# Kernel tuning notes

Measured on AMD Instinct MI355X. Metric: run time of the kernel, lower is better.

The kernel has to match this reference:

```python
import jax, jax.numpy as jnp
import numpy as np

RES = 64
NU = 0.002
DX = 2.0 * np.pi / RES
DT = 0.001
M1 = 12
M2 = 12
WIDTH = 32


def _central(x, axis, dx):
    # periodic central difference via roll (matches torch.roll semantics)
    return (jnp.roll(x, -1, axis) - jnp.roll(x, 1, axis)) / (2.0 * dx)


def _grad_module(u):
    # TurbulenceRCLN.compute_grad_u: central diff in x,y; j==2 branch is u*0.1 (kept faithfully)
    g0 = _central(u, 2, DX)
    g1 = _central(u, 3, DX)
    g2 = u * 0.1
    return jnp.stack([g0, g1, g2], axis=2)  # (B,3,3,N,N,N) indexed [b,i,j]


def _grad_solver(u):
    # NavierStokesSolver._compute_gradient: true central differences in all 3 dirs
    return jnp.stack([_central(u, 2 + j, DX) for j in range(3)], axis=2)


def _laplacian(u):
    lap = jnp.zeros_like(u)
    for ax in (2, 3, 4):
        lap = lap + (jnp.roll(u, -1, ax) - 2.0 * u + jnp.roll(u, 1, ax)) / (DX * DX)
    return lap


def _div_tau(tau):
    # tau: (B,3,3,N,N,N); div_i = sum_j d tau_ij / dx_j
    return sum(_central(tau[:, :, j], 2 + j, DX) for j in range(3))


def _spectral_conv(x, w1, w2):
    # x: (B,C,N,N); w1/w2: (C,C,M1,M2,2) real/imag
    N = x.shape[-1]
    xft = jnp.fft.rfft2(x)  # (B,C,N,N//2+1) complex
    w1c = w1[..., 0] + 1j * w1[..., 1]
    w2c = w2[..., 0] + 1j * w2[..., 1]
    a = jnp.einsum('bixy,ioxy->boxy', xft[:, :, :M1, :M2], w1c)
    b = jnp.einsum('bixy,ioxy->boxy', xft[:, :, -M1:, :M2], w2c)
    out = jnp.zeros_like(xft).at[:, :, :M1, :M2].set(a).at[:, :, -M1:, :M2].set(b)
    return jnp.fft.irfft2(out, s=(N, N))


def _fno2d(x, fc0_w, fc0_b, spec_w1, spec_w2, conv_w, conv_b, fc1_w, fc1_b, fc2_w, fc2_b):
    h = jnp.einsum('bcxy,cd->bdxy', x, fc0_w) + fc0_b[None, :, None, None]
    for l in range(4):
        s = _spectral_conv(h, spec_w1[l], spec_w2[l])
        w = jnp.einsum('bcxy,co->boxy', h, conv_w[l]) + conv_b[l][None, :, None, None]
        h = s + w
        if l < 3:
            h = jax.nn.gelu(h)
    h = jax.nn.gelu(jnp.einsum('bcxy,cd->bdxy', h, fc1_w) + fc1_b[None, :, None, None])
    return jnp.einsum('bcxy,cd->bdxy', h, fc2_w) + fc2_b[None, :, None, None]


def setup_inputs() -> dict:
    key = jax.random.key(0)
    ks = jax.random.split(key, 8)
    B = 16
    scale = 1.0 / (WIDTH * WIDTH)
    return {
        'velocity': jax.random.normal(ks[0], (B, 3, RES, RES, RES), jnp.float32),
        'fc0_w': jax.random.normal(ks[1], (10, WIDTH), jnp.float32) * 0.1,
        'fc0_b': jnp.zeros((WIDTH,), jnp.float32),
        'spec_w1': jax.random.normal(ks[2], (4, WIDTH, WIDTH, M1, M2, 2), jnp.float32) * scale,
        'spec_w2': jax.random.normal(ks[3], (4, WIDTH, WIDTH, M1, M2, 2), jnp.float32) * scale,
        'conv_w': jax.random.normal(ks[4], (4, WIDTH, WIDTH), jnp.float32) * 0.1,
        'conv_b': jnp.zeros((4, WIDTH), jnp.float32),
        'fc1_w': jax.random.normal(ks[5], (WIDTH, 128), jnp.float32) * 0.1,
        'fc1_b': jnp.zeros((128,), jnp.float32),
        'fc2_w': jax.random.normal(ks[6], (128, 6), jnp.float32) * 0.1,
        'fc2_b': jnp.zeros((6,), jnp.float32),
    }


def reference(velocity, fc0_w, fc0_b, spec_w1, spec_w2, conv_w, conv_b, fc1_w, fc1_b, fc2_w, fc2_b):
    B = velocity.shape[0]
    N = RES
    # --- soft-shell closure input ---
    grad_u = _grad_module(velocity)                                   # (B,3,3,N,N,N)
    S = 0.5 * (grad_u + jnp.swapaxes(grad_u, 1, 2))
    S_mag = jnp.sqrt(2.0 * jnp.sum(S * S, axis=(1, 2), keepdims=True))  # (B,1,1,N,N,N)
    g_slice = grad_u[:, :, :, :, N // 2, :].reshape(B, 9, N, N)        # 9 grad channels at mid-plane
    s_slice = S_mag[:, :, :, :, N // 2, :].reshape(B, 1, N, N)         # 1 strain-mag channel
    closure_in = jnp.concatenate([g_slice, s_slice], axis=1)          # (B,10,N,N)
    tau2d = _fno2d(closure_in, fc0_w, fc0_b, spec_w1, spec_w2, conv_w, conv_b,
                   fc1_w, fc1_b, fc2_w, fc2_b)                         # (B,6,N,N)
    t = jnp.broadcast_to(tau2d[..., None], (B, 6, N, N, N))           # expand along z
    # reconstruct symmetric stress tensor (B,3,3,N,N,N)
    row0 = jnp.stack([t[:, 0], t[:, 3], t[:, 4]], axis=1)
    row1 = jnp.stack([t[:, 3], t[:, 1], t[:, 5]], axis=1)
    row2 = jnp.stack([t[:, 4], t[:, 5], t[:, 2]], axis=1)
    tau_full = jnp.stack([row0, row1, row2], axis=1)
    # --- hard-core NS step ---
    g = _grad_solver(velocity)
    lap = _laplacian(velocity)
    convection = jnp.einsum('bixyz,bijxyz->bjxyz', velocity, g)
    div_tau = _div_tau(tau_full)
    return velocity + DT * (-convection + NU * lap + div_tau)
```

## Files before the change

### kernel.cpp

```cpp
#include <hip/hip_runtime.h>
#include <math.h>

#define NRES 64
#define NXY  4096
#define NVOL 262144
#define BB   16
#define WID  32
#define MM   12
#define R24  24

constexpr double DX_d   = 2.0 * 3.14159265358979323846 / 64.0;
constexpr float  INV2DX = (float)(1.0 / (2.0 * DX_d));
constexpr float  INVDX2 = (float)(1.0 / (DX_d * DX_d));
constexpr float  DT_c   = 0.001f;
constexpr float  NU_c   = 0.002f;

constexpr size_t OFF_FR  = 0;
constexpr size_t OFF_FI  = OFF_FR + (size_t)R24 * NRES;
constexpr size_t OFF_GR  = OFF_FI + (size_t)R24 * NRES;
constexpr size_t OFF_GI  = OFF_GR + (size_t)MM * NRES;
constexpr size_t OFF_CL  = OFF_GI + (size_t)MM * NRES;
constexpr size_t OFF_HA  = OFF_CL + (size_t)BB * 10 * NXY;
constexpr size_t OFF_HB  = OFF_HA + (size_t)BB * WID * NXY;
constexpr size_t OFF_T1R = OFF_HB + (size_t)BB * WID * NXY;
constexpr size_t OFF_T1I = OFF_T1R + (size_t)BB * WID * R24 * NRES;
constexpr size_t OFF_XR  = OFF_T1I + (size_t)BB * WID * R24 * NRES;
constexpr size_t OFF_XI  = OFF_XR + (size_t)BB * WID * R24 * MM;
constexpr size_t OFF_MR  = OFF_XI + (size_t)BB * WID * R24 * MM;
constexpr size_t OFF_MI  = OFF_MR + (size_t)BB * WID * R24 * MM;
constexpr size_t OFF_AR  = OFF_MI + (size_t)BB * WID * R24 * MM;
constexpr size_t OFF_AI  = OFF_AR + (size_t)BB * WID * MM * NRES;
constexpr size_t OFF_H1  = OFF_AI + (size_t)BB * WID * MM * NRES;
constexpr size_t OFF_TAU = OFF_H1 + (size_t)BB * 128 * NXY;
constexpr size_t OFF_FRT = OFF_TAU + (size_t)BB * 6 * NXY;
constexpr size_t OFF_FIT = OFF_FRT + (size_t)NRES * R24;

constexpr size_t OFF_SP  = OFF_H1;
constexpr size_t OFF_W1T = OFF_H1 + (size_t)BB * WID * NXY;
constexpr size_t OFF_CWT = OFF_W1T + 4096;
constexpr size_t OFF_W0T = OFF_CWT + 4096;

__device__ __forceinline__ float gelu_fast(float x) {
    float z = 0.79788456080286535588f * (x + 0.044715f * x * x * x);
    float e = __expf(2.0f * z);
    float t = 1.0f - 2.0f / (e + 1.0f);
    return 0.5f * x * (1.0f + t);
}

__global__ void k_setup(const float* __restrict__ fc1w, const float* __restrict__ convw,
                        const float* __restrict__ fc0w, float* __restrict__ ws) {
    int idx = blockIdx.x * 256 + threadIdx.x;
    if (idx < R24 * NRES) {
        int r = idx / NRES, x = idx % NRES;
        int kx = (r < MM) ? r : (r + 40);
        double ang = -2.0 * 3.14159265358979323846 * (double)(kx * x) / 64.0;
        float cr = (float)cos(ang), ci = (float)sin(ang);
        ws[OFF_FR + idx] = cr;
        ws[OFF_FI + idx] = ci;
        ws[OFF_FRT + (size_t)x * R24 + r] = cr;
        ws[OFF_FIT + (size_t)x * R24 + r] = ci;
    }
    if (idx < MM * NRES) {
        int ky = idx / NRES, y = idx % NRES;
        double ang = -2.0 * 3.14159265358979323846 * (double)(ky * y) / 64.0;
        ws[OFF_GR + idx] = (float)cos(ang);
        ws[OFF_GI + idx] = (float)sin(ang);
    }
    if (idx < 4096) {
        int c = idx >> 7, e = idx & 127;
        ws[OFF_W1T + (size_t)e * 32 + c] = fc1w[idx];
    } else if (idx < 8192) {
        int j = idx - 4096;
        int l = j >> 10, r = j & 1023;
        int c = r >> 5, o = r & 31;
        ws[OFF_CWT + (size_t)l * 1024 + o * 32 + c] = convw[j];
    } else if (idx < 8512) {
        int j = idx - 8192;
        int c = j >> 5, d = j & 31;
        ws[OFF_W0T + (size_t)d * 10 + c] = fc0w[j];
    }
}

__global__ void k_clfc0(const float* __restrict__ v, const float* __restrict__ w0t,
                        const float* __restrict__ bias, float* __restrict__ h) {
    __shared__ __align__(16) float sw[32 * 12];
    __shared__ float sb[32];
    int tid = threadIdx.x;
    for (int i = tid; i < 320; i += 256) {
        int d = i / 10, c = i % 10;
        sw[d * 12 + c] = w0t[i];
    }
    if (tid < 32) sb[tid] = bias[tid];
    __syncthreads();
    int idx = blockIdx.x * 256 + tid;
    int b = idx >> 10;
    int rr = idx & 1023;
    int x = rr >> 4, z0 = (rr & 15) * 4;
    int xp = (x + 1) & 63, xm = (x - 1) & 63;
    float4 cv[10];
    for (int i = 0; i < 3; i++) {
        const float* vb = v + (((size_t)(b * 3 + i)) << 18);
        float4 u4   = *(const float4*)(vb + (size_t)x  * 4096 + 32 * 64 + z0);
        float4 uxp4 = *(const float4*)(vb + (size_t)xp * 4096 + 32 * 64 + z0);
        float4 uxm4 = *(const float4*)(vb + (size_t)xm * 4096 + 32 * 64 + z0);
        float4 uyp4 = *(const float4*)(vb + (size_t)x  * 4096 + 33 * 64 + z0);
        float4 uym4 = *(const float4*)(vb + (size_t)x  * 4096 + 31 * 64 + z0);
        cv[i * 3 + 0] = make_float4((uxp4.x - uxm4.x) * INV2DX, (uxp4.y - uxm4.y) * INV2DX,
                                    (uxp4.z - uxm4.z) * INV2DX, (uxp4.w - uxm4.w) * INV2DX);
        cv[i * 3 + 1] = make_float4((uyp4.x - uym4.x) * INV2DX, (uyp4.y - uym4.y) * INV2DX,
                                    (uyp4.z - uym4.z) * INV2DX, (uyp4.w - uym4.w) * INV2DX);
        cv[i * 3 + 2] = make_float4(0.1f * u4.x, 0.1f * u4.y, 0.1f * u4.z, 0.1f * u4.w);
    }
    float4 ss = make_float4(0.f, 0.f, 0.f, 0.f);
    for (int i = 0; i < 3; i++)
        for (int j = 0; j < 3; j++) {
            float4 a = cv[i * 3 + j], bt = cv[j * 3 + i];
            float sx = 0.5f * (a.x + bt.x), sy = 0.5f * (a.y + bt.y);
            float sz = 0.5f * (a.z + bt.z), sw_ = 0.5f * (a.w + bt.w);
            ss.x += sx * sx; ss.y += sy * sy; ss.z += sz * sz; ss.w += sw_ * sw_;
        }
    cv[9] = make_float4(sqrtf(2.f * ss.x), sqrtf(2.f * ss.y),
                        sqrtf(2.f * ss.z), sqrtf(2.f * ss.w));
    float* hp = h + (size_t)b * WID * NXY + (size_t)x * 64 + z0;
#pragma unroll
    for (int d = 0; d < 32; d++) {
        float4 acc = make_float4(sb[d], sb[d], sb[d], sb[d]);
#pragma unroll
        for (int c = 0; c < 10; c++) {
            float w = sw[d * 12 + c];
            acc.x += w * cv[c].x; acc.y += w * cv[c].y;
            acc.z += w * cv[c].z; acc.w += w * cv[c].w;
        }
        *(float4*)(hp + (size_t)d * NXY) = acc;
    }
}

__global__ void k_fwd(const float* __restrict__ h, const float* __restrict__ ws,
                      float* __restrict__ xr, float* __restrict__ xi) {
    __shared__ __align__(16) float sh[4096];
    __shared__ float st1r[24 * 65];
    __shared__ float st1i[24 * 65];
    int tid = threadIdx.x;
    int bc = blockIdx.x;
    const float4* hp4 = (const float4*)(h + (size_t)bc * NXY);
    float4* sh4 = (float4*)sh;
#pragma unroll
    for (int i = 0; i < 4; i++) sh4[tid + 256 * i] = hp4[tid + 256 * i];
    __syncthreads();
    const float* FRT = ws + OFF_FRT;
    const float* FIT = ws + OFF_FIT;
#pragma unroll
    for (int it = 0; it < 6; it++) {
        int point = it * 256 + tid;
        int y = point & 63;
        int rr = __builtin_amdgcn_readfirstlane(point >> 6);
        float ar = 0.f, ai = 0.f;
#pragma unroll 16
        for (int x = 0; x < 64; x++) {
            float hv = sh[x * 64 + y];
            ar += hv * FRT[x * R24 + rr];
            ai += hv * FIT[x * R24 + rr];
        }
        st1r[rr * 65 + y] = ar;
        st1i[rr * 65 + y] = ai;
    }
    __syncthreads();
    const float* GR = ws + OFF_GR;
    const float* GI = ws + OFF_GI;
#pragma unroll
    for (int it = 0; it < 2; it++) {
        int point = it * 256 + tid;
        if (point < 288) {
            int r = point / 12, ky = point - r * 12;
            const float* Gr = GR + (size_t)ky * 64;
            const float* Gi = GI + (size_t)ky * 64;
            float ar = 0.f, ai = 0.f;
#pragma unroll 16
            for (int y = 0; y < 64; y++) {
                float a = st1r[r * 65 + y], b = st1i[r * 65 + y];
                float c = Gr[y], d = Gi[y];
                ar += a * c - b * d;
                ai += a * d + b * c;
            }
            xr[(size_t)bc * 288 + point] = ar;
            xi[(size_t)bc * 288 + point] = ai;
        }
    }
}

__global__ void k_specinv(const float* __restrict__ xr, const float* __restrict__ xi,
                          const float* __restrict__ w1, const float* __restrict__ w2,
                          const float* __restrict__ ws, float* __restrict__ sp) {
    __shared__ float sm_r[288];
    __shared__ float sm_i[288];
    __shared__ float sa_r[12 * 64];
    __shared__ float sa_i[12 * 64];
    int tid = threadIdx.x;
    int bo = blockIdx.x;
    int o = bo & 31, b = bo >> 5;
    for (int m = tid; m < 288; m += 256) {
        int r = m / 12;
        int kxy = (r < MM) ? m : (m - 144);
        const float* wp = ((r < MM) ? w1 : w2) + ((size_t)o * 144 + kxy) * 2;
        size_t xbase = (size_t)b * 32 * 288 + m;
        float ar = 0.f, ai = 0.f;
#pragma unroll 8
        for (int i = 0; i < 32; i++) {
            float a   = xr[xbase + (size_t)i * 288];
            float bb  = xi[xbase + (size_t)i * 288];
            float wr_ = wp[(size_t)i * 9216];
            float wi_ = wp[(size_t)i * 9216 + 1];
            ar += a * wr_ - bb * wi_;
            ai += a * wi_ + bb * wr_;
        }
        sm_r[m] = ar; sm_i[m] = ai;
    }
    __syncthreads();
    const float* FR = ws + OFF_FR;
    const float* FI = ws + OFF_FI;
#pragma unroll
    for (int it = 0; it < 3; it++) {
        int point = it * 256 + tid;
        int x = point & 63;
        int ky = __builtin_amdgcn_readfirstlane(point >> 6);
        float ar = 0.f, ai = 0.f;
#pragma unroll 8
        for (int r = 0; r < 24; r++) {
            float a = sm_r[r * 12 + ky], bb = sm_i[r * 12 + ky];
            float c = FR[r * 64 + x], d = FI[r * 64 + x];
            ar += a * c + bb * d;
            ai += bb * c - a * d;
        }
        sa_r[ky * 64 + x] = ar;
        sa_i[ky * 64 + x] = ai;
    }
    __syncthreads();
    const float* GR = ws + OFF_GR;
    const float* GI = ws + OFF_GI;
    float* spb = sp + (size_t)bo * NXY;
#pragma unroll
    for (int it = 0; it < 16; it++) {
        int px = it * 256 + tid;
        int y = px & 63;
        int x = __builtin_amdgcn_readfirstlane(px >> 6);
        float s = sa_r[x];
#pragma unroll
        for (int ky = 1; ky < 12; ky++) {
            float gr = GR[ky * 64 + y];
            float gi = GI[ky * 64 + y];
            s += 2.0f * (sa_r[ky * 64 + x] * gr + sa_i[ky * 64 + x] * gi);
        }
        spb[px] = s * (1.0f / 4096.0f);
    }
}

template <int DOGELU>
__global__ void k_convg(const float* __restrict__ sp, const float* __restrict__ hin,
                        const float* __restrict__ cwt, const float* __restrict__ cb,
                        float* __restrict__ hout) {
    __shared__ __align__(16) float scw[1024];
    __shared__ float scb[32];
    int tid = threadIdx.x;
#pragma unroll
    for (int i = 0; i < 4; i++) scw[tid + 256 * i] = cwt[tid + 256 * i];
    if (tid < 32) scb[tid] = cb[tid];
    __syncthreads();
    int wid = tid >> 6, lane = tid & 63;
    int pix = blockIdx.x * 64 + lane;
    int b = pix >> 12, p = pix & 4095;
    const float* hp = hin + (size_t)b * WID * NXY + p;
    float hv[32];
#pragma unroll
    for (int c = 0; c < 32; c++) hv[c] = hp[(size_t)c * NXY];
    const float* spp = sp + (size_t)b * WID * NXY + p;
    float* op = hout + (size_t)b * WID * NXY + p;
#pragma unroll
    for (int j = 0; j < 8; j++) {
        int o = wid * 8 + j;
        const float4* wr = (const float4*)&scw[o * 32];
        float a0 = 0.f, a1 = 0.f, a2 = 0.f, a3 = 0.f;
#pragma unroll
        for (int q = 0; q < 8; q += 4) {
            float4 w0 = wr[q], w1 = wr[q + 1], w2 = wr[q + 2], w3 = wr[q + 3];
            a0 += w0.x * hv[q * 4]      + w0.y * hv[q * 4 + 1]  + w0.z * hv[q * 4 + 2]  + w0.w * hv[q * 4 + 3];
            a1 += w1.x * hv[q * 4 + 4]  + w1.y * hv[q * 4 + 5]  + w1.z * hv[q * 4 + 6]  + w1.w * hv[q * 4 + 7];
            a2 += w2.x * hv[q * 4 + 8]  + w2.y * hv[q * 4 + 9]  + w2.z * hv[q * 4 + 10] + w2.w * hv[q * 4 + 11];
            a3 += w3.x * hv[q * 4 + 12] + w3.y * hv[q * 4 + 13] + w3.z * hv[q * 4 + 14] + w3.w * hv[q * 4 + 15];
        }
        float v = scb[o] + (a0 + a1) + (a2 + a3) + spp[(size_t)o * NXY];
        if (DOGELU) v = gelu_fast(v);
        op[(size_t)o * NXY] = v;
    }
}

__global__ void k_head(const float* __restrict__ h, const float* __restrict__ w1t,
                       const float* __restrict__ b1, const float* __restrict__ w2,
                       const float* __restrict__ b2, float* __restrict__ tau) {
    __shared__ __align__(16) float sw1[4096];
    __shared__ float sb1[128];
    __shared__ __align__(16) float sw2[128 * 8];
    __shared__ float red[4][6][64];
    int tid = threadIdx.x;
#pragma unroll
    for (int i = 0; i < 16; i++) sw1[tid + 256 * i] = w1t[tid + 256 * i];
    if (tid < 128) sb1[tid] = b1[tid];
    for (int i = tid; i < 768; i += 256) {
        int e = i / 6, t = i - e * 6;
        sw2[e * 8 + t] = w2[i];
    }
    __syncthreads();
    int wid = tid >> 6, lane = tid & 63;
    int pix = blockIdx.x * 64 + lane;
    int b = pix >> 12, p = pix & 4095;
    const float* hp = h + (size_t)b * WID * NXY + p;
    float hv[32];
#pragma unroll
    for (int c = 0; c < 32; c++) hv[c] = hp[(size_t)c * NXY];
    float acc[6] = {0.f, 0.f, 0.f, 0.f, 0.f, 0.f};
#pragma unroll
    for (int jj = 0; jj < 32; jj++) {
        int e = wid * 32 + jj;
        const float4* wr = (const float4*)&sw1[e * 32];
        float d0 = 0.f, d1 = 0.f, d2 = 0.f, d3 = 0.f;
#pragma unroll
        for (int q = 0; q < 8; q += 4) {
            float4 w0 = wr[q], w1 = wr[q + 1], w2_ = wr[q + 2], w3 = wr[q + 3];
            d0 += w0.x * hv[q * 4]      + w0.y * hv[q * 4 + 1]  + w0.z * hv[q * 4 + 2]  + w0.w * hv[q * 4 + 3];
            d1 += w1.x * hv[q * 4 + 4]  + w1.y * hv[q * 4 + 5]  + w1.z * hv[q * 4 + 6]  + w1.w * hv[q * 4 + 7];
            d2 += w2_.x * hv[q * 4 + 8] + w2_.y * hv[q * 4 + 9] + w2_.z * hv[q * 4 + 10]+ w2_.w * hv[q * 4 + 11];
            d3 += w3.x * hv[q * 4 + 12] + w3.y * hv[q * 4 + 13] + w3.z * hv[q * 4 + 14] + w3.w * hv[q * 4 + 15];
        }
        float d = sb1[e] + (d0 + d1) + (d2 + d3);
        float g = gelu_fast(d);
        const float4* w2r = (const float4*)&sw2[e * 8];
        float4 wa = w2r[0], wb = w2r[1];
        acc[0] += g * wa.x; acc[1] += g * wa.y; acc[2] += g * wa.z;
        acc[3] += g * wa.w; acc[4] += g * wb.x; acc[5] += g * wb.y;
    }
#pragma unroll
    for (int t = 0; t < 6; t++) red[wid][t][lane] = acc[t];
    __syncthreads();
    if (wid == 0) {
        float* tb = tau + (size_t)b * 6 * NXY + p;
#pragma unroll
        for (int t = 0; t < 6; t++)
            tb[(size_t)t * NXY] = red[0][t][lane] + red[1][t][lane] +
                                  red[2][t][lane] + red[3][t][lane] + b2[t];
    }
}

__global__ void k_ns(const float* __restrict__ v, const float* __restrict__ tau,
                     float* __restrict__ out) {
    int idx = blockIdx.x * 256 + threadIdx.x;
    int b = idx >> 16;
    int r = idx & 65535;
    int x = r >> 10;
    int y = (r >> 4) & 63;
    int z0 = (r & 15) * 4;
    int xp = (x + 1) & 63, xm = (x - 1) & 63;
    int yp = (y + 1) & 63, ym = (y - 1) & 63;
    int zm = (z0 - 1) & 63, zp = (z0 + 4) & 63;

    float4 u[3], gx[3], gy[3], gz[3], lap[3];
    for (int i = 0; i < 3; i++) {
        const float* vb = v + (((size_t)(b * 3 + i)) << 18);
        const float* row = vb + (size_t)x * 4096 + (size_t)y * 64;
        float4 c4   = *(const float4*)(row + z0);
        float  czm  = row[zm];
        float  czp  = row[zp];
        float4 xp4  = *(const float4*)(vb + (size_t)xp * 4096 + (size_t)y * 64 + z0);
        float4 xm4  = *(const float4*)(vb + (size_t)xm * 4096 + (size_t)y * 64 + z0);
        float4 yp4  = *(const float4*)(vb + (size_t)x * 4096 + (size_t)yp * 64 + z0);
        float4 ym4  = *(const float4*)(vb + (size_t)x * 4096 + (size_t)ym * 64 + z0);
        u[i] = c4;
        gx[i] = make_float4((xp4.x - xm4.x) * INV2DX, (xp4.y - xm4.y) * INV2DX,
                            (xp4.z - xm4.z) * INV2DX, (xp4.w - xm4.w) * INV2DX);
        gy[i] = make_float4((yp4.x - ym4.x) * INV2DX, (yp4.y - ym4.y) * INV2DX,
                            (yp4.z - ym4.z) * INV2DX, (yp4.w - ym4.w) * INV2DX);
        gz[i] = make_float4((c4.y - czm) * INV2DX, (c4.z - c4.x) * INV2DX,
                            (c4.w - c4.y) * INV2DX, (czp - c4.z) * INV2DX);
        lap[i] = make_float4(
            (xp4.x + xm4.x + yp4.x + ym4.x + czm  + c4.y - 6.f * c4.x) * INVDX2,
            (xp4.y + xm4.y + yp4.y + ym4.y + c4.x + c4.z - 6.f * c4.y) * INVDX2,
            (xp4.z + xm4.z + yp4.z + ym4.z + c4.y + c4.w - 6.f * c4.z) * INVDX2,
            (xp4.w + xm4.w + yp4.w + ym4.w + c4.z + czp  - 6.f * c4.w) * INVDX2);
    }
    const float* tb = tau + (size_t)b * 6 * NXY;
    int pxp = xp * 64 + y, pxm = xm * 64 + y, pyp = x * 64 + yp, pym = x * 64 + ym;
    float d0 = (tb[0 * NXY + pxp] - tb[0 * NXY + pxm]) * INV2DX +
               (tb[3 * NXY + pyp] - tb[3 * NXY + pym]) * INV2DX;
    float d1 = (tb[3 * NXY + pxp] - tb[3 * NXY + pxm]) * INV2DX +
               (tb[1 * NXY + pyp] - tb[1 * NXY + pym]) * INV2DX;
    float d2 = (tb[4 * NXY + pxp] - tb[4 * NXY + pxm]) * INV2DX +
               (tb[5 * NXY + pyp] - tb[5 * NXY + pym]) * INV2DX;

    size_t so = ((size_t)b * 3) * NVOL + (size_t)x * 4096 + (size_t)y * 64 + z0;
#pragma unroll
    for (int i = 0; i < 3; i++) {
        float dti = (i == 0) ? d0 : (i == 1) ? d1 : d2;
        float4 conv = make_float4(
            u[0].x * ((i==0)?gx[0].x:(i==1)?gy[0].x:gz[0].x) + u[1].x * ((i==0)?gx[1].x:(i==1)?gy[1].x:gz[1].x) + u[2].x * ((i==0)?gx[2].x:(i==1)?gy[2].x:gz[2].x),
            u[0].y * ((i==0)?gx[0].y:(i==1)?gy[0].y:gz[0].y) + u[1].y * ((i==0)?gx[1].y:(i==1)?gy[1].y:gz[1].y) + u[2].y * ((i==0)?gx[2].y:(i==1)?gy[2].y:gz[2].y),
            u[0].z * ((i==0)?gx[0].z:(i==1)?gy[0].z:gz[0].z) + u[1].z * ((i==0)?gx[1].z:(i==1)?gy[1].z:gz[1].z) + u[2].z * ((i==0)?gx[2].z:(i==1)?gy[2].z:gz[2].z),
            u[0].w * ((i==0)?gx[0].w:(i==1)?gy[0].w:gz[0].w) + u[1].w * ((i==0)?gx[1].w:(i==1)?gy[1].w:gz[1].w) + u[2].w * ((i==0)?gx[2].w:(i==1)?gy[2].w:gz[2].w));
        float4 res = make_float4(
            u[i].x + DT_c * (-conv.x + NU_c * lap[i].x + dti),
            u[i].y + DT_c * (-conv.y + NU_c * lap[i].y + dti),
            u[i].z + DT_c * (-conv.z + NU_c * lap[i].z + dti),
            u[i].w + DT_c * (-conv.w + NU_c * lap[i].w + dti));
        *(float4*)(out + so + (size_t)i * NVOL) = res;
    }
}

extern "C" void kernel_launch(void* const* d_in, const int* in_sizes, int n_in,
                              void* d_out, int out_size, void* d_ws, size_t ws_size,
                              hipStream_t stream) {
    const float* vel   = (const float*)d_in[0];
    const float* fc0w  = (const float*)d_in[1];
    const float* fc0b  = (const float*)d_in[2];
    const float* sw1   = (const float*)d_in[3];
    const float* sw2   = (const float*)d_in[4];
    const float* convw = (const float*)d_in[5];
    const float* convb = (const float*)d_in[6];
    const float* fc1w  = (const float*)d_in[7];
    const float* fc1b  = (const float*)d_in[8];
    const float* fc2w  = (const float*)d_in[9];
    const float* fc2b  = (const float*)d_in[10];
    float* ws  = (float*)d_ws;
    float* out = (float*)d_out;

    k_setup<<<34, 256, 0, stream>>>(fc1w, convw, fc0w, ws);
    k_clfc0<<<64, 256, 0, stream>>>(vel, ws + OFF_W0T, fc0b, ws + OFF_HA);

    float* hcur  = ws + OFF_HA;
    float* hnext = ws + OFF_HB;
    for (int l = 0; l < 4; l++) {
        const float* wl1 = sw1 + (size_t)l * WID * WID * MM * MM * 2;
        const float* wl2 = sw2 + (size_t)l * WID * WID * MM * MM * 2;
        const float* cwl = ws + OFF_CWT + (size_t)l * WID * WID;
        const float* cbl = convb + (size_t)l * WID;
        k_fwd<<<512, 256, 0, stream>>>(hcur, ws, ws + OFF_XR, ws + OFF_XI);
        k_specinv<<<512, 256, 0, stream>>>(ws + OFF_XR, ws + OFF_XI, wl1, wl2, ws, ws + OFF_SP);
        if (l < 3)
            k_convg<1><<<1024, 256, 0, stream>>>(ws + OFF_SP, hcur, cwl, cbl, hnext);
        else
            k_convg<0><<<1024, 256, 0, stream>>>(ws + OFF_SP, hcur, cwl, cbl, hnext);
        float* tmp = hcur; hcur = hnext; hnext = tmp;
    }

    k_head<<<1024, 256, 0, stream>>>(hcur, ws + OFF_W1T, fc1b, fc2w, fc2b, ws + OFF_TAU);
    k_ns<<<4096, 256, 0, stream>>>(vel, ws + OFF_TAU, out);
}
```

Baseline: 249.2 us.

## Register-block FNO kernels over four pixels and four modes per thread

The 1x1 conv and head kernels now have each thread handle four adjacent pixels using float4 loads and stores. Each shared-memory weight read is therefore reused four times, and the grid shrinks fourfold. The forward DFT computes four frequency rows per thread, reusing each loaded input value. The inverse DFT keeps the mode coefficients in registers and writes float4 outputs. The cost is much higher register use (128 floats for hv in conv and head), which lowers occupancy and leaves only 256 blocks, which may underfill the GPU.

After: 718.9 us. +188.5%, slower.

```diff
diff --git a/kernel.cpp b/kernel.cpp
--- a/kernel.cpp
+++ b/kernel.cpp
@@ -47,6 +47,10 @@
     return 0.5f * x * (1.0f + t);
 }
 
+__device__ __forceinline__ float4 gelu4(float4 v) {
+    return make_float4(gelu_fast(v.x), gelu_fast(v.y), gelu_fast(v.z), gelu_fast(v.w));
+}
+
 __global__ void k_setup(const float* __restrict__ fc1w, const float* __restrict__ convw,
                         const float* __restrict__ fc0w, float* __restrict__ ws) {
     int idx = blockIdx.x * 256 + threadIdx.x;
@@ -149,20 +153,26 @@
     __syncthreads();
     const float* FRT = ws + OFF_FRT;
     const float* FIT = ws + OFF_FIT;
-#pragma unroll
-    for (int it = 0; it < 6; it++) {
-        int point = it * 256 + tid;
-        int y = point & 63;
-        int rr = __builtin_amdgcn_readfirstlane(point >> 6);
-        float ar = 0.f, ai = 0.f;
-#pragma unroll 16
+    int y = tid & 63;
+    int wid = tid >> 6;
+    for (int g = wid; g < 6; g += 4) {
+        int r0 = __builtin_amdgcn_readfirstlane(g * 4);
+        float ar0 = 0.f, ai0 = 0.f, ar1 = 0.f, ai1 = 0.f;
+        float ar2 = 0.f, ai2 = 0.f, ar3 = 0.f, ai3 = 0.f;
+#pragma unroll 8
         for (int x = 0; x < 64; x++) {
             float hv = sh[x * 64 + y];
-            ar += hv * FRT[x * R24 + rr];
-            ai += hv * FIT[x * R24 + rr];
-        }
-        st1r[rr * 65 + y] = ar;
-        st1i[rr * 65 + y] = ai;
+            const float* fr = FRT + x * R24 + r0;
+            const float* fi = FIT + x * R24 + r0;
+            ar0 += hv * fr[0]; ai0 += hv * fi[0];
+            ar1 += hv * fr[1]; ai1 += hv * fi[1];
+            ar2 += hv * fr[2]; ai2 += hv * fi[2];
+            ar3 += hv * fr[3]; ai3 += hv * fi[3];
+        }
+        st1r[(r0 + 0) * 65 + y] = ar0; st1i[(r0 + 0) * 65 + y] = ai0;
+        st1r[(r0 + 1) * 65 + y] = ar1; st1i[(r0 + 1) * 65 + y] = ai1;
+        st1r[(r0 + 2) * 65 + y] = ar2; st1i[(r0 + 2) * 65 + y] = ai2;
+        st1r[(r0 + 3) * 65 + y] = ar3; st1i[(r0 + 3) * 65 + y] = ai3;
     }
     __syncthreads();
     const float* GR = ws + OFF_GR;
@@ -176,9 +186,9 @@
             const float* Gi = GI + (size_t)ky * 64;
             float ar = 0.f, ai = 0.f;
 #pragma unroll 16
-            for (int y = 0; y < 64; y++) {
-                float a = st1r[r * 65 + y], b = st1i[r * 65 + y];
-                float c = Gr[y], d = Gi[y];
+            for (int yy = 0; yy < 64; yy++) {
+                float a = st1r[r * 65 + yy], b = st1i[r * 65 + yy];
+                float c = Gr[yy], d = Gi[yy];
                 ar += a * c - b * d;
                 ai += a * d + b * c;
             }
@@ -238,19 +248,31 @@
     const float* GR = ws + OFF_GR;
     const float* GI = ws + OFF_GI;
     float* spb = sp + (size_t)bo * NXY;
-#pragma unroll
-    for (int it = 0; it < 16; it++) {
-        int px = it * 256 + tid;
-        int y = px & 63;
-        int x = __builtin_amdgcn_readfirstlane(px >> 6);
-        float s = sa_r[x];
+    int x = tid >> 2, ys = (tid & 3) * 16;
+    float a0 = sa_r[x];
+    float arv[11], aiv[11];
+#pragma unroll
+    for (int ky = 1; ky < 12; ky++) {
+        arv[ky - 1] = sa_r[ky * 64 + x];
+        aiv[ky - 1] = sa_i[ky * 64 + x];
+    }
+#pragma unroll
+    for (int j = 0; j < 4; j++) {
+        int y0 = ys + j * 4;
+        float4 s = make_float4(a0, a0, a0, a0);
 #pragma unroll
         for (int ky = 1; ky < 12; ky++) {
-            float gr = GR[ky * 64 + y];
-            float gi = GI[ky * 64 + y];
-            s += 2.0f * (sa_r[ky * 64 + x] * gr + sa_i[ky * 64 + x] * gi);
-        }
-        spb[px] = s * (1.0f / 4096.0f);
+            float4 g4r = *(const float4*)(GR + ky * 64 + y0);
+            float4 g4i = *(const float4*)(GI + ky * 64 + y0);
+            float ar = arv[ky - 1], ai = aiv[ky - 1];
+            s.x += 2.0f * (ar * g4r.x + ai * g4i.x);
+            s.y += 2.0f * (ar * g4r.y + ai * g4i.y);
+            s.z += 2.0f * (ar * g4r.z + ai * g4i.z);
+            s.w += 2.0f * (ar * g4r.w + ai * g4i.w);
+        }
+        s.x *= (1.0f / 4096.0f); s.y *= (1.0f / 4096.0f);
+        s.z *= (1.0f / 4096.0f); s.w *= (1.0f / 4096.0f);
+        *(float4*)(spb + (size_t)x * 64 + y0) = s;
     }
 }
 
@@ -266,30 +288,32 @@
     if (tid < 32) scb[tid] = cb[tid];
     __syncthreads();
     int wid = tid >> 6, lane = tid & 63;
-    int pix = blockIdx.x * 64 + lane;
-    int b = pix >> 12, p = pix & 4095;
+    int q = blockIdx.x * 64 + lane;
+    int b = q >> 10, p = (q & 1023) * 4;
     const float* hp = hin + (size_t)b * WID * NXY + p;
-    float hv[32];
-#pragma unroll
-    for (int c = 0; c < 32; c++) hv[c] = hp[(size_t)c * NXY];
+    float4 hv[32];
+#pragma unroll
+    for (int c = 0; c < 32; c++) hv[c] = *(const float4*)(hp + (size_t)c * NXY);
     const float* spp = sp + (size_t)b * WID * NXY + p;
     float* op = hout + (size_t)b * WID * NXY + p;
 #pragma unroll
     for (int j = 0; j < 8; j++) {
         int o = wid * 8 + j;
         const float4* wr = (const float4*)&scw[o * 32];
-        float a0 = 0.f, a1 = 0.f, a2 = 0.f, a3 = 0.f;
-#pragma unroll
-        for (int q = 0; q < 8; q += 4) {
-            float4 w0 = wr[q], w1 = wr[q + 1], w2 = wr[q + 2], w3 = wr[q + 3];
-            a0 += w0.x * hv[q * 4]      + w0.y * hv[q * 4 + 1]  + w0.z * hv[q * 4 + 2]  + w0.w * hv[q * 4 + 3];
-            a1 += w1.x * hv[q * 4 + 4]  + w1.y * hv[q * 4 + 5]  + w1.z * hv[q * 4 + 6]  + w1.w * hv[q * 4 + 7];
-            a2 += w2.x * hv[q * 4 + 8]  + w2.y * hv[q * 4 + 9]  + w2.z * hv[q * 4 + 10] + w2.w * hv[q * 4 + 11];
-            a3 += w3.x * hv[q * 4 + 12] + w3.y * hv[q * 4 + 13] + w3.z * hv[q * 4 + 14] + w3.w * hv[q * 4 + 15];
-        }
-        float v = scb[o] + (a0 + a1) + (a2 + a3) + spp[(size_t)o * NXY];
-        if (DOGELU) v = gelu_fast(v);
-        op[(size_t)o * NXY] = v;
+        float4 d = make_float4(scb[o], scb[o], scb[o], scb[o]);
+#pragma unroll
+        for (int q8 = 0; q8 < 8; q8++) {
+            float4 w = wr[q8];
+            float4 h0 = hv[q8 * 4], h1 = hv[q8 * 4 + 1], h2 = hv[q8 * 4 + 2], h3 = hv[q8 * 4 + 3];
+            d.x += w.x * h0.x + w.y * h1.x + w.z * h2.x + w.w * h3.x;
+            d.y += w.x * h0.y + w.y * h1.y + w.z * h2.y + w.w * h3.y;
+            d.z += w.x * h0.z + w.y * h1.z + w.z * h2.z + w.w * h3.z;
+            d.w += w.x * h0.w + w.y * h1.w + w.z * h2.w + w.w * h3.w;
+        }
+        float4 spv = *(const float4*)(spp + (size_t)o * NXY);
+        float4 v = make_float4(d.x + spv.x, d.y + spv.y, d.z + spv.z, d.w + spv.w);
+        if (DOGELU) v = gelu4(v);
+        *(float4*)(op + (size_t)o * NXY) = v;
     }
 }
 
@@ -299,7 +323,7 @@
     __shared__ __align__(16) float sw1[4096];
     __shared__ float sb1[128];
     __shared__ __align__(16) float sw2[128 * 8];
-    __shared__ float red[4][6][64];
+    __shared__ __align__(16) float4 red[4][6][64];
     int tid = threadIdx.x;
 #pragma unroll
     for (int i = 0; i < 16; i++) sw1[tid + 256 * i] = w1t[tid + 256 * i];
@@ -310,32 +334,38 @@
     }
     __syncthreads();
     int wid = tid >> 6, lane = tid & 63;
-    int pix = blockIdx.x * 64 + lane;
-    int b = pix >> 12, p = pix & 4095;
+    int q = blockIdx.x * 64 + lane;
+    int b = q >> 10, p = (q & 1023) * 4;
     const float* hp = h + (size_t)b * WID * NXY + p;
-    float hv[32];
-#pragma unroll
-    for (int c = 0; c < 32; c++) hv[c] = hp[(size_t)c * NXY];
-    float acc[6] = {0.f, 0.f, 0.f, 0.f, 0.f, 0.f};
+    float4 hv[32];
+#pragma unroll
+    for (int c = 0; c < 32; c++) hv[c] = *(const float4*)(hp + (size_t)c * NXY);
+    float4 acc[6];
+#pragma unroll
+    for (int t = 0; t < 6; t++) acc[t] = make_float4(0.f, 0.f, 0.f, 0.f);
 #pragma unroll
     for (int jj = 0; jj < 32; jj++) {
         int e = wid * 32 + jj;
         const float4* wr = (const float4*)&sw1[e * 32];
-        float d0 = 0.f, d1 = 0.f, d2 = 0.f, d3 = 0.f;
-#pragma unroll
-        for (int q = 0; q < 8; q += 4) {
-            float4 w0 = wr[q], w1 = wr[q + 1], w2_ = wr[q + 2], w3 = wr[q + 3];
-            d0 += w0.x * hv[q * 4]      + w0.y * hv[q * 4 + 1]  + w0.z * hv[q * 4 + 2]  + w0.w * hv[q * 4 + 3];
-            d1 += w1.x * hv[q * 4 + 4]  + w1.y * hv[q * 4 + 5]  + w1.z * hv[q * 4 + 6]  + w1.w * hv[q * 4 + 7];
-            d2 += w2_.x * hv[q * 4 + 8] + w2_.y * hv[q * 4 + 9] + w2_.z * hv[q * 4 + 10]+ w2_.w * hv[q * 4 + 11];
-            d3 += w3.x * hv[q * 4 + 12] + w3.y * hv[q * 4 + 13] + w3.z * hv[q * 4 + 14] + w3.w * hv[q * 4 + 15];
-        }
-        float d = sb1[e] + (d0 + d1) + (d2 + d3);
-        float g = gelu_fast(d);
+        float4 d = make_float4(sb1[e], sb1[e], sb1[e], sb1[e]);
+#pragma unroll
+        for (int q8 = 0; q8 < 8; q8++) {
+            float4 w = wr[q8];
+            float4 h0 = hv[q8 * 4], h1 = hv[q8 * 4 + 1], h2 = hv[q8 * 4 + 2], h3 = hv[q8 * 4 + 3];
+            d.x += w.x * h0.x + w.y * h1.x + w.z * h2.x + w.w * h3.x;
+            d.y += w.x * h0.y + w.y * h1.y + w.z * h2.y + w.w * h3.y;
+            d.z += w.x * h0.z + w.y * h1.z + w.z * h2.z + w.w * h3.z;
+            d.w += w.x * h0.w + w.y * h1.w + w.z * h2.w + w.w * h3.w;
+        }
+        float4 g = gelu4(d);
         const float4* w2r = (const float4*)&sw2[e * 8];
         float4 wa = w2r[0], wb = w2r[1];
-        acc[0] += g * wa.x; acc[1] += g * wa.y; acc[2] += g * wa.z;
-        acc[3] += g * wa.w; acc[4] += g * wb.x; acc[5] += g * wb.y;
+        acc[0].x += g.x * wa.x; acc[0].y += g.y * wa.x; acc[0].z += g.z * wa.x; acc[0].w += g.w * wa.x;
+        acc[1].x += g.x * wa.y; acc[1].y += g.y * wa.y; acc[1].z += g.z * wa.y; acc[1].w += g.w * wa.y;
+        acc[2].x += g.x * wa.z; acc[2].y += g.y * wa.z; acc[2].z += g.z * wa.z; acc[2].w += g.w * wa.z;
+        acc[3].x += g.x * wa.w; acc[3].y += g.y * wa.w; acc[3].z += g.z * wa.w; acc[3].w += g.w * wa.w;
+        acc[4].x += g.x * wb.x; acc[4].y += g.y * wb.x; acc[4].z += g.z * wb.x; acc[4].w += g.w * wb.x;
+        acc[5].x += g.x * wb.y; acc[5].y += g.y * wb.y; acc[5].z += g.z * wb.y; acc[5].w += g.w * wb.y;
     }
 #pragma unroll
     for (int t = 0; t < 6; t++) red[wid][t][lane] = acc[t];
@@ -343,9 +373,16 @@
     if (wid == 0) {
         float* tb = tau + (size_t)b * 6 * NXY + p;
 #pragma unroll
-        for (int t = 0; t < 6; t++)
-            tb[(size_t)t * NXY] = red[0][t][lane] + red[1][t][lane] +
-                                  red[2][t][lane] + red[3][t][lane] + b2[t];
+        for (int t = 0; t < 6; t++) {
+            float4 r0 = red[0][t][lane], r1 = red[1][t][lane];
+            float4 r2 = red[2][t][lane], r3 = red[3][t][lane];
+            float bv = b2[t];
+            float4 s = make_float4(r0.x + r1.x + r2.x + r3.x + bv,
+                                   r0.y + r1.y + r2.y + r3.y + bv,
+                                   r0.z + r1.z + r2.z + r3.z + bv,
+                                   r0.w + r1.w + r2.w + r3.w + bv);
+            *(float4*)(tb + (size_t)t * NXY) = s;
+        }
     }
 }
 
@@ -442,12 +479,12 @@
         k_fwd<<<512, 256, 0, stream>>>(hcur, ws, ws + OFF_XR, ws + OFF_XI);
         k_specinv<<<512, 256, 0, stream>>>(ws + OFF_XR, ws + OFF_XI, wl1, wl2, ws, ws + OFF_SP);
         if (l < 3)
-            k_convg<1><<<1024, 256, 0, stream>>>(ws + OFF_SP, hcur, cwl, cbl, hnext);
+            k_convg<1><<<256, 256, 0, stream>>>(ws + OFF_SP, hcur, cwl, cbl, hnext);
         else
-            k_convg<0><<<1024, 256, 0, stream>>>(ws + OFF_SP, hcur, cwl, cbl, hnext);
+            k_convg<0><<<256, 256, 0, stream>>>(ws + OFF_SP, hcur, cwl, cbl, hnext);
         float* tmp = hcur; hcur = hnext; hnext = tmp;
     }
 
-    k_head<<<1024, 256, 0, stream>>>(hcur, ws + OFF_W1T, fc1b, fc2w, fc2b, ws + OFF_TAU);
+    k_head<<<256, 256, 0, stream>>>(hcur, ws + OFF_W1T, fc1b, fc2w, fc2b, ws + OFF_TAU);
     k_ns<<<4096, 256, 0, stream>>>(vel, ws + OFF_TAU, out);
 }
```
